# Kernel tuning notes

Measured on AMD Instinct MI355X. Metric: run time of the kernel, lower is better.

## Reference

```python
import jax, jax.numpy as jnp
import numpy as np

B = 16384      # batch
N = 128        # number of DNPU nodes (experts)
I = 3          # data electrodes per node
C = 4          # control electrodes per node
E = I + C      # total electrodes = 7
H = 90         # surrogate-model hidden width
L = 3          # number of extra hidden layers


def setup_inputs() -> dict:
    key = jax.random.key(0)
    ks = jax.random.split(key, 8)
    s_in = 1.0 / np.sqrt(E)
    s_h = 1.0 / np.sqrt(H)
    return {
        "x": jax.random.normal(ks[0], (B, N * I), dtype=jnp.float32),
        "controls": jax.random.uniform(ks[1], (N, C), dtype=jnp.float32, minval=-1.2, maxval=0.6),
        "W_in": jax.random.normal(ks[2], (N, E, H), dtype=jnp.float32) * s_in,
        "b_in": jax.random.normal(ks[3], (N, H), dtype=jnp.float32) * 0.1,
        "W_hid": jax.random.normal(ks[4], (L, N, H, H), dtype=jnp.float32) * s_h,
        "b_hid": jax.random.normal(ks[5], (L, N, H), dtype=jnp.float32) * 0.1,
        "W_out": jax.random.normal(ks[6], (N, H), dtype=jnp.float32) * s_h,
        "b_out": jax.random.normal(ks[7], (N,), dtype=jnp.float32) * 0.1,
    }


def reference(x, controls, W_in, b_in, W_hid, b_hid, W_out, b_out):
    # DNPU_Layer: partition x into N chunks of I, each node merges its data
    # electrodes with its learned control voltages into a 7-electrode vector,
    # evaluates the shared surrogate MLP with per-node parameters, outputs 1
    # current per node; results are concatenated along dim 1 -> [B, N].
    b = x.shape[0]
    xd = x.reshape(b, N, I)                                   # partition_input
    ctrl = jnp.broadcast_to(controls[None], (b, N, C))        # per-node controls
    e = jnp.concatenate([xd, ctrl], axis=-1)                  # [B, N, E]
    h = jax.nn.relu(jnp.einsum('bne,neh->bnh', e, W_in) + b_in)
    for l in range(L):  # fixed small layer count
        h = jax.nn.relu(jnp.einsum('bnh,nhk->bnk', h, W_hid[l]) + b_hid[l])
    out = jnp.einsum('bnh,nh->bn', h, W_out) + b_out          # [B, N]
    return out
```

## Files before the change

### kernel.cpp

```cpp
#include <hip/hip_runtime.h>
#include <stdint.h>

namespace {
constexpr int kB  = 16384;
constexpr int kN  = 128;
constexpr int kI  = 3;
constexpr int kC  = 4;
constexpr int kH  = 90;
constexpr int kL  = 3;
constexpr int BT  = 64;
constexpr int KP  = 96;
constexpr int LDP = 104;
constexpr int TILE_USH = 18 * 512;
constexpr size_t WT_BYTES = (size_t)4 * kN * TILE_USH * 2;
constexpr size_t WOUT_OFF = WT_BYTES;
}

typedef __attribute__((ext_vector_type(8))) short bf16x8;
typedef __attribute__((ext_vector_type(4))) float f32x4;

__device__ __forceinline__ uint32_t pack_bf16(float lo, float hi) {
#if __has_builtin(__builtin_amdgcn_cvt_pk_bf16_f32)
  auto r = __builtin_amdgcn_cvt_pk_bf16_f32(lo, hi);
  union { decltype(r) v; uint32_t u; } c; c.v = r; return c.u;
#else
  union { float f; uint32_t i; } a, b; a.f = lo; b.f = hi;
  uint32_t ua = a.i + 0x7FFFu + ((a.i >> 16) & 1u);
  uint32_t ub = b.i + 0x7FFFu + ((b.i >> 16) & 1u);
  return (ua >> 16) | (ub & 0xFFFF0000u);
#endif
}
__device__ __forceinline__ ushort f2bf(float f) {
  union { float f; uint32_t i; } v; v.f = f;
  uint32_t u = v.i + 0x7FFFu + ((v.i >> 16) & 1u);
  return (ushort)(u >> 16);
}

__global__ __launch_bounds__(256) void prep_weights(
    const float* __restrict__ W_in, const float* __restrict__ b_in,
    const float* __restrict__ W_hid, const float* __restrict__ b_hid,
    const float* __restrict__ W_out, const float* __restrict__ b_out,
    ushort* __restrict__ wt, float* __restrict__ wo)
{
  const int tid = threadIdx.x;
  if (blockIdx.x >= 4 * kN) {
    int base = (int)(blockIdx.x - 4 * kN) * 3072;
    for (int t = 0; t < 12; ++t) {
      int idx = base + t * 256 + tid;
      int node = idx / KP, j = idx % KP;
      float v = 0.f;
      if (j < kH)       v = W_out[node * kH + j];
      else if (j == kH) v = b_out[node];
      wo[idx] = v;
    }
    return;
  }
  __shared__ float ldsw[kH][kH + 1];
  __shared__ float ldsb[kH];
  const int node  = blockIdx.x & (kN - 1);
  const int layer = blockIdx.x >> 7;
  const int ksrc  = (layer == 0) ? (kI + kC) : kH;
  const float* src;
  const float* bsrc;
  if (layer == 0) { src = W_in + (size_t)node * (kI + kC) * kH; bsrc = b_in + (size_t)node * kH; }
  else {
    int l = layer - 1;
    src  = W_hid + (size_t)(l * kN + node) * kH * kH;
    bsrc = b_hid + (size_t)(l * kN + node) * kH;
  }
  for (int idx = tid; idx < ksrc * kH; idx += 256)
    ldsw[idx / kH][idx % kH] = src[idx];
  if (tid < kH) ldsb[tid] = bsrc[tid];
  __syncthreads();
  ushort* dst = wt + (size_t)blockIdx.x * TILE_USH;
  const int nush = (layer == 0) ? 6 * 512 : TILE_USH;
  for (int idx = tid; idx < nush; idx += 256) {
    int fb = idx >> 9, lane = (idx >> 3) & 63, i = idx & 7;
    int mt = fb % 6, ks = fb / 6;
    int j = mt * 16 + (lane & 15);
    int k = ks * 32 + (lane >> 4) * 8 + i;
    float v = 0.f;
    if (j < kH) {
      if (k < ksrc)       v = ldsw[k][j];
      else if (k == ksrc) v = ldsb[j];
    }
    dst[idx] = f2bf(v);
  }
}

__global__ __launch_bounds__(64, 3) void dnpu_kernel(
    const float* __restrict__ x, const float* __restrict__ controls,
    const ushort* __restrict__ wt, const float* __restrict__ wo,
    float* __restrict__ out)
{
  __shared__ __align__(16) ushort hbuf[BT][LDP];

  const int lane = threadIdx.x;
  const int node = (int)(blockIdx.x & 127);
  const int m0   = (int)(blockIdx.x >> 7) * BT;
  const int quad = lane >> 4;
  const int l16  = lane & 15;

  {
    const float* xr = x + (size_t)(m0 + lane) * (kN * kI) + node * kI;
    float x0 = xr[0], x1 = xr[1], x2 = xr[2];
    float c0 = controls[node * kC + 0], c1 = controls[node * kC + 1];
    float c2 = controls[node * kC + 2], c3 = controls[node * kC + 3];
    uint4 v;
    v.x = pack_bf16(x0, x1);
    v.y = pack_bf16(x2, c0);
    v.z = pack_bf16(c1, c2);
    v.w = pack_bf16(c3, 1.0f);
    *(uint4*)&hbuf[lane][0]  = v;
    uint4 z = {0, 0, 0, 0};
    *(uint4*)&hbuf[lane][8]  = z;
    *(uint4*)&hbuf[lane][16] = z;
    *(uint4*)&hbuf[lane][24] = z;
  }

  f32x4 acc[6][4];
  auto zero_acc = [&]() {
#pragma unroll
    for (int mt = 0; mt < 6; ++mt)
#pragma unroll
      for (int nt = 0; nt < 4; ++nt)
        acc[mt][nt] = (f32x4){0.f, 0.f, 0.f, 0.f};
  };

  auto run_gemm = [&](const ushort* tl, int ksteps) {
    for (int ks = 0; ks < ksteps; ++ks) {
      bf16x8 bfr[4];
#pragma unroll
      for (int nt = 0; nt < 4; ++nt)
        bfr[nt] = *(const bf16x8*)&hbuf[nt * 16 + l16][ks * 32 + quad * 8];
      bf16x8 afr[6];
#pragma unroll
      for (int mt = 0; mt < 6; ++mt)
        afr[mt] = *(const bf16x8*)&tl[(size_t)(ks * 6 + mt) * 512 + lane * 8];
#pragma unroll
      for (int mt = 0; mt < 6; ++mt)
#pragma unroll
        for (int nt = 0; nt < 4; ++nt)
          acc[mt][nt] = __builtin_amdgcn_mfma_f32_16x16x32_bf16(afr[mt], bfr[nt], acc[mt][nt], 0, 0, 0);
    }
  };

  auto write_h = [&]() {
#pragma unroll
    for (int mt = 0; mt < 6; ++mt)
#pragma unroll
      for (int nt = 0; nt < 4; ++nt) {
        float v0 = fmaxf(acc[mt][nt][0], 0.f);
        float v1 = fmaxf(acc[mt][nt][1], 0.f);
        float v2 = fmaxf(acc[mt][nt][2], 0.f);
        float v3 = fmaxf(acc[mt][nt][3], 0.f);
        if (mt == 5 && quad == 2) v2 = 1.0f;
        uint2 p;
        p.x = pack_bf16(v0, v1);
        p.y = pack_bf16(v2, v3);
        *(uint2*)&hbuf[nt * 16 + l16][mt * 16 + quad * 4] = p;
      }
  };

  const ushort* t0 = wt + (size_t)(0 * kN + node) * TILE_USH;
  zero_acc();
  run_gemm(t0, 1);

#pragma unroll
  for (int l = 0; l < kL; ++l) {
    write_h();
    zero_acc();
    run_gemm(wt + (size_t)((l + 1) * kN + node) * TILE_USH, 3);
  }

  {
    float4 wof[6];
#pragma unroll
    for (int mt = 0; mt < 6; ++mt)
      wof[mt] = *(const float4*)&wo[node * KP + mt * 16 + quad * 4];
    float s0 = 0.f, s1 = 0.f, s2 = 0.f, s3 = 0.f;
#pragma unroll
    for (int mt = 0; mt < 6; ++mt) {
      float w0 = wof[mt].x, w1 = wof[mt].y, w2 = wof[mt].z, w3 = wof[mt].w;
#pragma unroll
      for (int nt = 0; nt < 4; ++nt) {
        float h0 = fmaxf(acc[mt][nt][0], 0.f);
        float h1 = fmaxf(acc[mt][nt][1], 0.f);
        float h2 = fmaxf(acc[mt][nt][2], 0.f);
        float h3 = fmaxf(acc[mt][nt][3], 0.f);
        if (mt == 5 && quad == 2) h2 = 1.0f;
        float p = h0 * w0 + h1 * w1 + h2 * w2 + h3 * w3;
        if (nt == 0) s0 += p; else if (nt == 1) s1 += p;
        else if (nt == 2) s2 += p; else s3 += p;
      }
    }
    s0 += __shfl_xor(s0, 16); s0 += __shfl_xor(s0, 32);
    s1 += __shfl_xor(s1, 16); s1 += __shfl_xor(s1, 32);
    s2 += __shfl_xor(s2, 16); s2 += __shfl_xor(s2, 32);
    s3 += __shfl_xor(s3, 16); s3 += __shfl_xor(s3, 32);
    float r = (quad == 0) ? s0 : (quad == 1) ? s1 : (quad == 2) ? s2 : s3;
    int col = quad * 16 + l16;
    out[(size_t)(m0 + col) * kN + node] = r;
  }
}

extern "C" void kernel_launch(void* const* d_in, const int* in_sizes, int n_in,
                              void* d_out, int out_size, void* d_ws, size_t ws_size,
                              hipStream_t stream) {
  const float* x        = (const float*)d_in[0];
  const float* controls = (const float*)d_in[1];
  const float* W_in     = (const float*)d_in[2];
  const float* b_in     = (const float*)d_in[3];
  const float* W_hid    = (const float*)d_in[4];
  const float* b_hid    = (const float*)d_in[5];
  const float* W_out    = (const float*)d_in[6];
  const float* b_out    = (const float*)d_in[7];
  float* out = (float*)d_out;

  ushort* wt = (ushort*)d_ws;
  float*  wo = (float*)((char*)d_ws + WOUT_OFF);

  hipLaunchKernelGGL(prep_weights, dim3(4 * kN + 4), dim3(256), 0, stream,
                     W_in, b_in, W_hid, b_hid, W_out, b_out, wt, wo);

  dim3 grid((kB / BT) * kN);
  hipLaunchKernelGGL(dnpu_kernel, grid, dim3(BT), 0, stream,
                     x, controls, wt, wo, out);
}
```

Measured before the change: 252.2 us.

## Pre-transpose input to node-major bf16, swizzle LDS, and transpose output separately

The prep kernel now also transposes x into a node-major bf16 buffer, so the main kernel can build the first-layer MFMA B operand directly in registers with coalesced loads and skip the LDS staging. The hidden-activation LDS buffer gets an XOR swizzle to cut bank conflicts, and the k-loop is fully unrolled. Output is written node-major (coalesced) into a workspace buffer and then reordered by a new transpose kernel. This adds an extra launch and extra global traffic for the x and output transposes in exchange for coalesced access in the main kernel.

```diff
diff --git a/kernel.cpp b/kernel.cpp
--- a/kernel.cpp
+++ b/kernel.cpp
@@ -13,7 +13,9 @@
 constexpr int LDP = 104;
 constexpr int TILE_USH = 18 * 512;
 constexpr size_t WT_BYTES = (size_t)4 * kN * TILE_USH * 2;
-constexpr size_t WOUT_OFF = WT_BYTES;
+constexpr size_t WO_OFF   = WT_BYTES;
+constexpr size_t XK_OFF   = WO_OFF + (size_t)kN * KP * 4;
+constexpr size_t OT_OFF   = XK_OFF + (size_t)kN * kI * kB * 2;
 }
 
 typedef __attribute__((ext_vector_type(8))) short bf16x8;
@@ -36,15 +38,55 @@
   return (ushort)(u >> 16);
 }
 
-__global__ __launch_bounds__(256) void prep_weights(
+__device__ __forceinline__ int swz(int blk, int l16) {
+  return (blk < 8) ? (blk ^ (l16 & 7)) : (8 + ((blk & 3) ^ (l16 & 3)));
+}
+
+__global__ __launch_bounds__(256) void prep_kernel(
+    const float* __restrict__ x,
     const float* __restrict__ W_in, const float* __restrict__ b_in,
     const float* __restrict__ W_hid, const float* __restrict__ b_hid,
     const float* __restrict__ W_out, const float* __restrict__ b_out,
-    ushort* __restrict__ wt, float* __restrict__ wo)
+    ushort* __restrict__ wt, float* __restrict__ wo, ushort* __restrict__ xk)
 {
+  __shared__ float smem[kH * (kH + 1) + kH];
   const int tid = threadIdx.x;
-  if (blockIdx.x >= 4 * kN) {
-    int base = (int)(blockIdx.x - 4 * kN) * 3072;
+  const int bid = blockIdx.x;
+
+  if (bid < 4 * kN) {
+    float* ldsw = smem;
+    float* ldsb = smem + kH * (kH + 1);
+    const int node  = bid & (kN - 1);
+    const int layer = bid >> 7;
+    const int ksrc  = (layer == 0) ? (kI + kC) : kH;
+    const float* src;
+    const float* bsrc;
+    if (layer == 0) { src = W_in + (size_t)node * (kI + kC) * kH; bsrc = b_in + (size_t)node * kH; }
+    else {
+      int l = layer - 1;
+      src  = W_hid + (size_t)(l * kN + node) * kH * kH;
+      bsrc = b_hid + (size_t)(l * kN + node) * kH;
+    }
+    for (int idx = tid; idx < ksrc * kH; idx += 256)
+      ldsw[(idx / kH) * (kH + 1) + (idx % kH)] = src[idx];
+    if (tid < kH) ldsb[tid] = bsrc[tid];
+    __syncthreads();
+    ushort* dst = wt + (size_t)bid * TILE_USH;
+    const int nush = (layer == 0) ? 6 * 512 : TILE_USH;
+    for (int idx = tid; idx < nush; idx += 256) {
+      int fb = idx >> 9, lane = (idx >> 3) & 63, i = idx & 7;
+      int mt = fb % 6, ks = fb / 6;
+      int j = mt * 16 + (lane & 15);
+      int k = ks * 32 + (lane >> 4) * 8 + i;
+      float v = 0.f;
+      if (j < kH) {
+        if (k < ksrc)       v = ldsw[k * (kH + 1) + j];
+        else if (k == ksrc) v = ldsb[j];
+      }
+      dst[idx] = f2bf(v);
+    }
+  } else if (bid < 4 * kN + 4) {
+    int base = (bid - 4 * kN) * 3072;
     for (int t = 0; t < 12; ++t) {
       int idx = base + t * 256 + tid;
       int node = idx / KP, j = idx % KP;
@@ -53,45 +95,27 @@
       else if (j == kH) v = b_out[node];
       wo[idx] = v;
     }
-    return;
-  }
-  __shared__ float ldsw[kH][kH + 1];
-  __shared__ float ldsb[kH];
-  const int node  = blockIdx.x & (kN - 1);
-  const int layer = blockIdx.x >> 7;
-  const int ksrc  = (layer == 0) ? (kI + kC) : kH;
-  const float* src;
-  const float* bsrc;
-  if (layer == 0) { src = W_in + (size_t)node * (kI + kC) * kH; bsrc = b_in + (size_t)node * kH; }
-  else {
-    int l = layer - 1;
-    src  = W_hid + (size_t)(l * kN + node) * kH * kH;
-    bsrc = b_hid + (size_t)(l * kN + node) * kH;
-  }
-  for (int idx = tid; idx < ksrc * kH; idx += 256)
-    ldsw[idx / kH][idx % kH] = src[idx];
-  if (tid < kH) ldsb[tid] = bsrc[tid];
-  __syncthreads();
-  ushort* dst = wt + (size_t)blockIdx.x * TILE_USH;
-  const int nush = (layer == 0) ? 6 * 512 : TILE_USH;
-  for (int idx = tid; idx < nush; idx += 256) {
-    int fb = idx >> 9, lane = (idx >> 3) & 63, i = idx & 7;
-    int mt = fb % 6, ks = fb / 6;
-    int j = mt * 16 + (lane & 15);
-    int k = ks * 32 + (lane >> 4) * 8 + i;
-    float v = 0.f;
-    if (j < kH) {
-      if (k < ksrc)       v = ldsw[k][j];
-      else if (k == ksrc) v = ldsb[j];
-    }
-    dst[idx] = f2bf(v);
+  } else {
+    int xb = bid - (4 * kN + 4);
+    int b0 = (xb & 255) * 64;
+    int c0 = (xb >> 8) * 96;
+    float* lds = smem;
+    for (int idx = tid; idx < 64 * 96; idx += 256) {
+      int r = idx / 96, c = idx % 96;
+      lds[r * 97 + c] = x[(size_t)(b0 + r) * (kN * kI) + c0 + c];
+    }
+    __syncthreads();
+    for (int idx = tid; idx < 96 * 64; idx += 256) {
+      int nk = idx >> 6, b = idx & 63;
+      xk[(size_t)(c0 + nk) * kB + b0 + b] = f2bf(lds[b * 97 + nk]);
+    }
   }
 }
 
 __global__ __launch_bounds__(64, 3) void dnpu_kernel(
-    const float* __restrict__ x, const float* __restrict__ controls,
+    const ushort* __restrict__ xk, const float* __restrict__ controls,
     const ushort* __restrict__ wt, const float* __restrict__ wo,
-    float* __restrict__ out)
+    float* __restrict__ outT)
 {
   __shared__ __align__(16) ushort hbuf[BT][LDP];
 
@@ -101,23 +125,6 @@
   const int quad = lane >> 4;
   const int l16  = lane & 15;
 
-  {
-    const float* xr = x + (size_t)(m0 + lane) * (kN * kI) + node * kI;
-    float x0 = xr[0], x1 = xr[1], x2 = xr[2];
-    float c0 = controls[node * kC + 0], c1 = controls[node * kC + 1];
-    float c2 = controls[node * kC + 2], c3 = controls[node * kC + 3];
-    uint4 v;
-    v.x = pack_bf16(x0, x1);
-    v.y = pack_bf16(x2, c0);
-    v.z = pack_bf16(c1, c2);
-    v.w = pack_bf16(c3, 1.0f);
-    *(uint4*)&hbuf[lane][0]  = v;
-    uint4 z = {0, 0, 0, 0};
-    *(uint4*)&hbuf[lane][8]  = z;
-    *(uint4*)&hbuf[lane][16] = z;
-    *(uint4*)&hbuf[lane][24] = z;
-  }
-
   f32x4 acc[6][4];
   auto zero_acc = [&]() {
 #pragma unroll
@@ -127,27 +134,51 @@
         acc[mt][nt] = (f32x4){0.f, 0.f, 0.f, 0.f};
   };
 
-  auto run_gemm = [&](const ushort* tl, int ksteps) {
-    for (int ks = 0; ks < ksteps; ++ks) {
-      bf16x8 bfr[4];
+  bf16x8 bfr0[4];
+  {
+    const ushort cb0 = f2bf(controls[node * kC + 0]);
+    const ushort cb1 = f2bf(controls[node * kC + 1]);
+    const ushort cb2 = f2bf(controls[node * kC + 2]);
+    const ushort cb3 = f2bf(controls[node * kC + 3]);
+    if (quad == 0) {
+      const ushort* x0p = xk + (size_t)(node * kI + 0) * kB + m0 + l16;
+      const ushort* x1p = xk + (size_t)(node * kI + 1) * kB + m0 + l16;
+      const ushort* x2p = xk + (size_t)(node * kI + 2) * kB + m0 + l16;
+#pragma unroll
+      for (int nt = 0; nt < 4; ++nt) {
+        union { ushort s[8]; bf16x8 v; } f;
+        f.s[0] = x0p[nt * 16]; f.s[1] = x1p[nt * 16]; f.s[2] = x2p[nt * 16];
+        f.s[3] = cb0; f.s[4] = cb1; f.s[5] = cb2; f.s[6] = cb3;
+        f.s[7] = 0x3F80;
+        bfr0[nt] = f.v;
+      }
+    } else {
 #pragma unroll
       for (int nt = 0; nt < 4; ++nt)
-        bfr[nt] = *(const bf16x8*)&hbuf[nt * 16 + l16][ks * 32 + quad * 8];
-      bf16x8 afr[6];
-#pragma unroll
-      for (int mt = 0; mt < 6; ++mt)
-        afr[mt] = *(const bf16x8*)&tl[(size_t)(ks * 6 + mt) * 512 + lane * 8];
-#pragma unroll
-      for (int mt = 0; mt < 6; ++mt)
-#pragma unroll
-        for (int nt = 0; nt < 4; ++nt)
-          acc[mt][nt] = __builtin_amdgcn_mfma_f32_16x16x32_bf16(afr[mt], bfr[nt], acc[mt][nt], 0, 0, 0);
-    }
-  };
+        bfr0[nt] = (bf16x8){0,0,0,0,0,0,0,0};
+    }
+  }
+
+  zero_acc();
+  {
+    const ushort* tl = wt + (size_t)(0 * kN + node) * TILE_USH;
+    bf16x8 afr[6];
+#pragma unroll
+    for (int mt = 0; mt < 6; ++mt)
+      afr[mt] = *(const bf16x8*)&tl[(size_t)mt * 512 + lane * 8];
+#pragma unroll
+    for (int mt = 0; mt < 6; ++mt)
+#pragma unroll
+      for (int nt = 0; nt < 4; ++nt)
+        acc[mt][nt] = __builtin_amdgcn_mfma_f32_16x16x32_bf16(afr[mt], bfr0[nt], acc[mt][nt], 0, 0, 0);
+  }
 
   auto write_h = [&]() {
 #pragma unroll
-    for (int mt = 0; mt < 6; ++mt)
+    for (int mt = 0; mt < 6; ++mt) {
+      const int blk  = 2 * mt + (quad >> 1);
+      const int blk2 = swz(blk, l16);
+      const int coff = blk2 * 8 + (quad & 1) * 4;
 #pragma unroll
       for (int nt = 0; nt < 4; ++nt) {
         float v0 = fmaxf(acc[mt][nt][0], 0.f);
@@ -158,19 +189,37 @@
         uint2 p;
         p.x = pack_bf16(v0, v1);
         p.y = pack_bf16(v2, v3);
-        *(uint2*)&hbuf[nt * 16 + l16][mt * 16 + quad * 4] = p;
+        *(uint2*)&hbuf[nt * 16 + l16][coff] = p;
       }
+    }
   };
 
-  const ushort* t0 = wt + (size_t)(0 * kN + node) * TILE_USH;
-  zero_acc();
-  run_gemm(t0, 1);
+  auto run_gemm = [&](const ushort* tl) {
+#pragma unroll
+    for (int ks = 0; ks < 3; ++ks) {
+      const int blk  = 4 * ks + quad;
+      const int blk2 = swz(blk, l16);
+      bf16x8 bfr[4];
+#pragma unroll
+      for (int nt = 0; nt < 4; ++nt)
+        bfr[nt] = *(const bf16x8*)&hbuf[nt * 16 + l16][blk2 * 8];
+      bf16x8 afr[6];
+#pragma unroll
+      for (int mt = 0; mt < 6; ++mt)
+        afr[mt] = *(const bf16x8*)&tl[(size_t)(ks * 6 + mt) * 512 + lane * 8];
+#pragma unroll
+      for (int mt = 0; mt < 6; ++mt)
+#pragma unroll
+        for (int nt = 0; nt < 4; ++nt)
+          acc[mt][nt] = __builtin_amdgcn_mfma_f32_16x16x32_bf16(afr[mt], bfr[nt], acc[mt][nt], 0, 0, 0);
+    }
+  };
 
 #pragma unroll
   for (int l = 0; l < kL; ++l) {
     write_h();
     zero_acc();
-    run_gemm(wt + (size_t)((l + 1) * kN + node) * TILE_USH, 3);
+    run_gemm(wt + (size_t)((l + 1) * kN + node) * TILE_USH);
   }
 
   {
@@ -181,7 +230,6 @@
     float s0 = 0.f, s1 = 0.f, s2 = 0.f, s3 = 0.f;
 #pragma unroll
     for (int mt = 0; mt < 6; ++mt) {
-      float w0 = wof[mt].x, w1 = wof[mt].y, w2 = wof[mt].z, w3 = wof[mt].w;
 #pragma unroll
       for (int nt = 0; nt < 4; ++nt) {
         float h0 = fmaxf(acc[mt][nt][0], 0.f);
@@ -189,7 +237,7 @@
         float h2 = fmaxf(acc[mt][nt][2], 0.f);
         float h3 = fmaxf(acc[mt][nt][3], 0.f);
         if (mt == 5 && quad == 2) h2 = 1.0f;
-        float p = h0 * w0 + h1 * w1 + h2 * w2 + h3 * w3;
+        float p = h0 * wof[mt].x + h1 * wof[mt].y + h2 * wof[mt].z + h3 * wof[mt].w;
         if (nt == 0) s0 += p; else if (nt == 1) s1 += p;
         else if (nt == 2) s2 += p; else s3 += p;
       }
@@ -199,8 +247,28 @@
     s2 += __shfl_xor(s2, 16); s2 += __shfl_xor(s2, 32);
     s3 += __shfl_xor(s3, 16); s3 += __shfl_xor(s3, 32);
     float r = (quad == 0) ? s0 : (quad == 1) ? s1 : (quad == 2) ? s2 : s3;
-    int col = quad * 16 + l16;
-    out[(size_t)(m0 + col) * kN + node] = r;
+    outT[(size_t)node * kB + m0 + lane] = r;
+  }
+}
+
+__global__ __launch_bounds__(256) void transpose_out(
+    const float* __restrict__ ot, float* __restrict__ out)
+{
+  __shared__ float t[64][65];
+  const int b0 = (int)(blockIdx.x & 255) * 64;
+  const int n0 = (int)(blockIdx.x >> 8) * 64;
+  const int c  = threadIdx.x & 63;
+  const int r4 = threadIdx.x >> 6;
+#pragma unroll
+  for (int i = 0; i < 16; ++i) {
+    int n = r4 + i * 4;
+    t[n][c] = ot[(size_t)(n0 + n) * kB + b0 + c];
+  }
+  __syncthreads();
+#pragma unroll
+  for (int i = 0; i < 16; ++i) {
+    int b = r4 + i * 4;
+    out[(size_t)(b0 + b) * kN + n0 + c] = t[c][b];
   }
 }
 
@@ -218,12 +286,16 @@
   float* out = (float*)d_out;
 
   ushort* wt = (ushort*)d_ws;
-  float*  wo = (float*)((char*)d_ws + WOUT_OFF);
-
-  hipLaunchKernelGGL(prep_weights, dim3(4 * kN + 4), dim3(256), 0, stream,
-                     W_in, b_in, W_hid, b_hid, W_out, b_out, wt, wo);
+  float*  wo = (float*)((char*)d_ws + WO_OFF);
+  ushort* xk = (ushort*)((char*)d_ws + XK_OFF);
+  float*  ot = (float*)((char*)d_ws + OT_OFF);
+
+  hipLaunchKernelGGL(prep_kernel, dim3(4 * kN + 4 + 1024), dim3(256), 0, stream,
+                     x, W_in, b_in, W_hid, b_hid, W_out, b_out, wt, wo, xk);
 
   dim3 grid((kB / BT) * kN);
   hipLaunchKernelGGL(dnpu_kernel, grid, dim3(BT), 0, stream,
-                     x, controls, wt, wo, out);
-}
+                     xk, controls, wt, wo, ot);
+
+  hipLaunchKernelGGL(transpose_out, dim3(512), dim3(256), 0, stream, ot, out);
+}
```

Measured after the change: 272.2 us. 7.9% more time.
